# Kernel optimization log

Measured on AMD Instinct MI355X. Metric: run time of the kernel, lower is better.

The kernel has to match this reference:

```python
import jax, jax.numpy as jnp
import numpy as np

TW = 25; HID = 128; LAYERS = 6; SPATIAL = 1; NVAR = 1
TMAX = 4.0; TMIN = 0.0; RES_T = 250.0; DOM = 16.0
N = 65536; B = 8; E = 393216
EPS = 1e-5


def swish(x):
    return x * jax.nn.sigmoid(x)


def _forward(u, x_pos, t_pos, variables,
             emb_w1, emb_b1, emb_w2, emb_b2,
             m1_w, m1_b, m2_w, m2_b,
             u1_w, u1_b, u2_w, u2_b,
             c1_w, c1_b, c2_w, c2_b,
             edge_index, batch):
    t_norm = t_pos / TMAX                       # [N]
    pos = x_pos / DOM                           # [N, 1] normalized by domain extent
    node_in = jnp.concatenate([u, pos, t_norm[:, None], variables], axis=-1)
    f = swish(node_in @ emb_w1 + emb_b1)
    f = swish(f @ emb_w2 + emb_b2)              # [N, HID]

    var_all = jnp.concatenate([t_norm[:, None], variables], axis=-1)  # [N, NVAR+1]
    src, dst = edge_index[0], edge_index[1]     # PyG: x_j = x[src], x_i = x[dst]
    du = u[dst] - u[src]                        # [E, TW]
    dp = pos[dst] - pos[src]                    # [E, SPATIAL]
    v_i = var_all[dst]                          # [E, NVAR+1]

    ones_e = jnp.ones((E,), f.dtype)
    deg = jnp.maximum(jax.ops.segment_sum(ones_e, dst, num_segments=N), 1.0)
    ones_n = jnp.ones((N,), f.dtype)
    gcount = jnp.maximum(jax.ops.segment_sum(ones_n, batch, num_segments=B), 1.0)

    for l in range(LAYERS):
        # message: concat(x_i, x_j, u_i-u_j, pos_i-pos_j, vars_i) -> 2-layer MLP
        m = jnp.concatenate([f[dst], f[src], du, dp, v_i], axis=-1)  # [E, 284]
        m = swish(m @ m1_w[l] + m1_b[l])
        m = swish(m @ m2_w[l] + m2_b[l])
        agg = jax.ops.segment_sum(m, dst, num_segments=N) / deg[:, None]  # mean aggr
        # update: concat(x, message, vars) -> 2-layer MLP, residual (in==out)
        h = jnp.concatenate([f, agg, var_all], axis=-1)  # [N, 258]
        h = swish(h @ u1_w[l] + u1_b[l])
        h = swish(h @ u2_w[l] + u2_b[l])
        h = f + h
        # InstanceNorm over nodes within each graph, per feature (no affine)
        mean = jax.ops.segment_sum(h, batch, num_segments=B) / gcount[:, None]
        var = jax.ops.segment_sum(h * h, batch, num_segments=B) / gcount[:, None] - mean * mean
        f = (h - mean[batch]) * jax.lax.rsqrt(var[batch] + EPS)

    # output CNN head over feature axis: [N, 1, HID] -> [N, 1, TW]
    y = jax.lax.conv_general_dilated(f[:, None, :], c1_w, (3,), 'VALID',
                                     dimension_numbers=('NCH', 'OIH', 'NCH'))
    y = swish(y + c1_b[None, :, None])
    y = jax.lax.conv_general_dilated(y, c2_w, (1,), 'VALID',
                                     dimension_numbers=('NCH', 'OIH', 'NCH'))
    diff = y[:, 0, :] + c2_b[0]                 # [N, TW]

    dt = jnp.cumsum(jnp.full((TW,), (TMAX - TMIN) / RES_T, dtype=f.dtype))
    out = u[:, -1][:, None] + dt[None, :] * diff
    return out


def setup_inputs() -> dict:
    key = jax.random.key(0)
    keys = iter(jax.random.split(key, 128))

    def lin(i, o):
        s = 1.0 / np.sqrt(i)
        w = jax.random.uniform(next(keys), (i, o), jnp.float32, -s, s)
        b = jax.random.uniform(next(keys), (o,), jnp.float32, -s, s)
        return w, b

    def stacked(i, o):
        ws, bs = zip(*[lin(i, o) for _ in range(LAYERS)])
        return jnp.stack(ws), jnp.stack(bs)

    def conv(o, i, k):
        s = 1.0 / np.sqrt(i * k)
        w = jax.random.uniform(next(keys), (o, i, k), jnp.float32, -s, s)
        b = jax.random.uniform(next(keys), (o,), jnp.float32, -s, s)
        return w, b

    emb_w1, emb_b1 = lin(TW + SPATIAL + 1 + NVAR, HID)
    emb_w2, emb_b2 = lin(HID, HID)
    m1_w, m1_b = stacked(2 * HID + TW + SPATIAL + NVAR + 1, HID)
    m2_w, m2_b = stacked(HID, HID)
    u1_w, u1_b = stacked(2 * HID + NVAR + 1, HID)
    u2_w, u2_b = stacked(HID, HID)
    c1_w, c1_b = conv(8, 1, 16)
    c2_w, c2_b = conv(1, 8, 14)

    u = jax.random.normal(next(keys), (N, TW), jnp.float32)
    x_pos = jax.random.uniform(next(keys), (N, SPATIAL), jnp.float32) * DOM
    t_pos = jax.random.uniform(next(keys), (N,), jnp.float32) * TMAX
    variables = jax.random.normal(next(keys), (N, NVAR), jnp.float32)
    edge_index = jax.random.randint(next(keys), (2, E), 0, N, jnp.int32)
    batch = jnp.sort(jax.random.randint(next(keys), (N,), 0, B, jnp.int32))

    return {'u': u, 'x_pos': x_pos, 't_pos': t_pos, 'variables': variables,
            'edge_index': edge_index, 'batch': batch,
            'emb_w1': emb_w1, 'emb_b1': emb_b1, 'emb_w2': emb_w2, 'emb_b2': emb_b2,
            'm1_w': m1_w, 'm1_b': m1_b, 'm2_w': m2_w, 'm2_b': m2_b,
            'u1_w': u1_w, 'u1_b': u1_b, 'u2_w': u2_w, 'u2_b': u2_b,
            'c1_w': c1_w, 'c1_b': c1_b, 'c2_w': c2_w, 'c2_b': c2_b}


def reference(u, x_pos, t_pos, variables, edge_index, batch,
              emb_w1, emb_b1, emb_w2, emb_b2,
              m1_w, m1_b, m2_w, m2_b,
              u1_w, u1_b, u2_w, u2_b,
              c1_w, c1_b, c2_w, c2_b):
    return _forward(u, x_pos, t_pos, variables,
                    emb_w1, emb_b1, emb_w2, emb_b2,
                    m1_w, m1_b, m2_w, m2_b,
                    u1_w, u1_b, u2_w, u2_b,
                    c1_w, c1_b, c2_w, c2_b,
                    edge_index, batch)
```

## Files before the change

kernel.cpp:

```cpp
#include <hip/hip_runtime.h>
#include <hip/hip_bf16.h>

#define N_NODES 65536
#define N_EDGES 393216
#define NB 8
#define HID 128
#define TW 25
#define LAYERS 6
#define BGRAPH 8
#define EPSF 1e-5f
#define TILE_E 128

typedef __attribute__((ext_vector_type(8))) short bf16x8;
typedef __attribute__((ext_vector_type(4))) float f32x4;

__device__ __forceinline__ float swishf(float x) {
    return x / (1.0f + __expf(-x));
}

__device__ __forceinline__ unsigned short f2bf(float x) {
    unsigned int u = __float_as_uint(x);
    u += 0x7fffu + ((u >> 16) & 1u);
    return (unsigned short)(u >> 16);
}

__device__ __forceinline__ unsigned int cvtpk2bf(float lo, float hi) {
    unsigned int r;
    asm("v_cvt_pk_bf16_f32 %0, %1, %2" : "=v"(r) : "v"(lo), "v"(hi));
    return r;
}

__device__ __forceinline__ unsigned short f2bf_rne(float x) {
    unsigned int r;
    asm("v_cvt_pk_bf16_f32 %0, %1, %2" : "=v"(r) : "v"(x), "v"(x));
    return (unsigned short)r;
}

__device__ __forceinline__ float bf2f(unsigned short v) {
    return __uint_as_float(((unsigned int)v) << 16);
}

__global__ void gcount_kernel(const int* __restrict__ batch, float* __restrict__ gcount) {
    int b = threadIdx.x;
    if (b >= BGRAPH) return;
    auto lb = [&](int key) {
        int lo = 0, hi = N_NODES;
        while (lo < hi) { int mid = (lo + hi) >> 1; if (batch[mid] < key) lo = mid + 1; else hi = mid; }
        return lo;
    };
    int c = lb(b + 1) - lb(b);
    gcount[b] = c > 0 ? (float)c : 1.0f;
}

__global__ void count_kernel(const int* __restrict__ ei, int* __restrict__ cnt) {
    int e = blockIdx.x * 256 + threadIdx.x;
    if (e < N_EDGES) atomicAdd(&cnt[ei[N_EDGES + e]], 1);
}

__global__ __launch_bounds__(256) void block_sum_kernel(const int* __restrict__ cnt, int* __restrict__ bsum) {
    __shared__ int s[256];
    int t = threadIdx.x;
    s[t] = cnt[blockIdx.x * 256 + t];
    __syncthreads();
    for (int st = 128; st > 0; st >>= 1) {
        if (t < st) s[t] += s[t + st];
        __syncthreads();
    }
    if (t == 0) bsum[blockIdx.x] = s[0];
}

__global__ __launch_bounds__(256) void scan_bsum_kernel(const int* __restrict__ bsum, int* __restrict__ bpref) {
    __shared__ int s[256];
    int t = threadIdx.x;
    int orig = bsum[t];
    s[t] = orig;
    __syncthreads();
    for (int st = 1; st < 256; st <<= 1) {
        int v = (t >= st) ? s[t - st] : 0;
        __syncthreads();
        s[t] += v;
        __syncthreads();
    }
    bpref[t] = s[t] - orig;
}

__global__ __launch_bounds__(256) void offsets_kernel(const int* __restrict__ cnt, const int* __restrict__ bpref,
                                                      int* __restrict__ cursor) {
    __shared__ int s[256];
    int t = threadIdx.x;
    int base = blockIdx.x * 256;
    int orig = cnt[base + t];
    s[t] = orig;
    __syncthreads();
    for (int st = 1; st < 256; st <<= 1) {
        int v = (t >= st) ? s[t - st] : 0;
        __syncthreads();
        s[t] += v;
        __syncthreads();
    }
    cursor[base + t] = s[t] - orig + bpref[blockIdx.x];
}

__global__ void scatter_kernel(const int* __restrict__ ei, int* __restrict__ cursor,
                               int* __restrict__ src_s, int* __restrict__ dst_s) {
    int e = blockIdx.x * 256 + threadIdx.x;
    if (e >= N_EDGES) return;
    int d = ei[N_EDGES + e];
    int pos = atomicAdd(&cursor[d], 1);
    src_s[pos] = ei[e];
    dst_s[pos] = d;
}

__global__ void w2bf_kernel(const float* __restrict__ m2_w, unsigned short* __restrict__ W2T) {
    int idx = blockIdx.x * 256 + threadIdx.x;
    int l = idx >> 14;
    int rem = idx & 16383;
    int n = rem >> 7, k = rem & 127;
    W2T[idx] = f2bf(m2_w[l * 16384 + k * HID + n]);
}

__global__ void w1t_kernel(const float* __restrict__ m1_w, unsigned short* __restrict__ wAB) {
    int idx = blockIdx.x * 256 + threadIdx.x;
    int l = idx / (2 * 128 * 160);
    int rem = idx % (2 * 128 * 160);
    int pass = rem / (128 * 160);
    int o = (rem % (128 * 160)) / 160;
    int k = rem % 160;
    const float* M = m1_w + (size_t)l * 284 * 128;
    float v;
    if (k < 128) {
        v = M[(pass ? 128 + k : k) * 128 + o];
    } else {
        int ku = k - 128;
        if (ku < 25) v = M[(256 + ku) * 128 + o];
        else if (ku == 25) v = M[281 * 128 + o];
        else if (ku == 26) v = M[282 * 128 + o];
        else if (ku == 27) v = M[283 * 128 + o];
        else v = 0.0f;
        if (pass) v = (ku <= 25) ? -v : 0.0f;
    }
    wAB[idx] = f2bf(v);
}

__global__ void u1t_kernel(const float* __restrict__ u1_w, unsigned short* __restrict__ U1T) {
    int idx = blockIdx.x * 256 + threadIdx.x;
    int l = idx >> 15;
    int o = (idx >> 8) & 127;
    int k = idx & 255;
    U1T[idx] = f2bf(u1_w[(size_t)l * 258 * 128 + k * 128 + o]);
}

__global__ void u2t_kernel(const float* __restrict__ u2_w, unsigned short* __restrict__ U2T) {
    int idx = blockIdx.x * 256 + threadIdx.x;
    int l = idx >> 14;
    int o = (idx >> 7) & 127;
    int k = idx & 127;
    U2T[idx] = f2bf(u2_w[(size_t)l * 16384 + k * 128 + o]);
}

__global__ void wemb_kernel(const float* __restrict__ ew1, const float* __restrict__ ew2,
                            unsigned short* __restrict__ we1T, unsigned short* __restrict__ we2T) {
    int idx = blockIdx.x * 256 + threadIdx.x;
    if (idx < 4096) {
        int o = idx >> 5, k = idx & 31;
        we1T[idx] = f2bf(k < 28 ? ew1[k * HID + o] : 0.0f);
    } else {
        int j = idx - 4096;
        int o = j >> 7, k = j & 127;
        we2T[j] = f2bf(ew2[k * HID + o]);
    }
}

__global__ void xin_kernel(const float* __restrict__ u, const float* __restrict__ xpos,
                           const float* __restrict__ tpos, const float* __restrict__ vars,
                           unsigned short* __restrict__ xin) {
    int idx = blockIdx.x * 256 + threadIdx.x;
    int n = idx >> 5, k = idx & 31;
    float v;
    if (k < 25) v = u[n * TW + k];
    else if (k == 25) v = xpos[n] * (1.0f / 16.0f);
    else if (k == 26) v = tpos[n] * 0.25f;
    else if (k == 27) v = vars[n];
    else v = 0.0f;
    xin[idx] = f2bf(v);
}

__device__ __forceinline__ void abv_tail(
    const bf16x8 (&afr)[2][5], int nb, int lr, int lk,
    const unsigned short* __restrict__ wA, const unsigned short* __restrict__ wB,
    const float* __restrict__ b1,
    unsigned short* __restrict__ A_bf, unsigned short* __restrict__ Bv_bf)
{
    #pragma unroll 1
    for (int pass = 0; pass < 2; ++pass) {
        const unsigned short* Wp = pass ? wB : wA;
        unsigned short* Op = pass ? Bv_bf : A_bf;
        #pragma unroll 1
        for (int cc = 0; cc < 4; ++cc) {
            f32x4 acc[2][2];
            #pragma unroll
            for (int rt = 0; rt < 2; ++rt)
                #pragma unroll
                for (int cf2 = 0; cf2 < 2; ++cf2)
                    acc[rt][cf2] = (f32x4){0.0f, 0.0f, 0.0f, 0.0f};
            #pragma unroll
            for (int cf2 = 0; cf2 < 2; ++cf2) {
                const unsigned short* wrow = Wp + ((cc * 2 + cf2) * 16 + lr) * 160 + lk * 8;
                #pragma unroll
                for (int ks = 0; ks < 5; ++ks) {
                    bf16x8 bfr = *reinterpret_cast<const bf16x8*>(wrow + ks * 32);
                    acc[0][cf2] = __builtin_amdgcn_mfma_f32_16x16x32_bf16(afr[0][ks], bfr, acc[0][cf2], 0, 0, 0);
                    acc[1][cf2] = __builtin_amdgcn_mfma_f32_16x16x32_bf16(afr[1][ks], bfr, acc[1][cf2], 0, 0, 0);
                }
            }
            #pragma unroll
            for (int cf2 = 0; cf2 < 2; ++cf2) {
                int col = (cc * 2 + cf2) * 16 + lr;
                float bb = pass ? 0.0f : b1[col];
                #pragma unroll
                for (int rt = 0; rt < 2; ++rt) {
                    #pragma unroll
                    for (int j = 0; j < 4; ++j) {
                        int row = nb + rt * 16 + lk * 4 + j;
                        Op[(size_t)row * HID + col] = f2bf_rne(acc[rt][cf2][j] + bb);
                    }
                }
            }
        }
    }
}

__global__ __launch_bounds__(256) void emb_abv_kernel(
    const unsigned short* __restrict__ xin_bf,
    const unsigned short* __restrict__ we1T, const float* __restrict__ eb1,
    const unsigned short* __restrict__ we2T, const float* __restrict__ eb2,
    const unsigned short* __restrict__ wA, const unsigned short* __restrict__ wB,
    const float* __restrict__ b1,
    unsigned short* __restrict__ f_bf,
    unsigned short* __restrict__ A_bf, unsigned short* __restrict__ Bv_bf)
{
    __shared__ unsigned short q_lds[4 * 32 * HID];
    const int tid = threadIdx.x;
    const int w = tid >> 6, l = tid & 63;
    const int lr = l & 15, lk = l >> 4;
    const int nb = blockIdx.x * 128 + w * 32;
    char* qbase = reinterpret_cast<char*>(q_lds) + w * 8192;

    bf16x8 xfr[2];
    #pragma unroll
    for (int rt = 0; rt < 2; ++rt)
        xfr[rt] = *reinterpret_cast<const bf16x8*>(xin_bf + (size_t)(nb + rt * 16 + lr) * 32 + lk * 8);

    #pragma unroll 1
    for (int cc = 0; cc < 4; ++cc) {
        f32x4 acc1[2][2];
        #pragma unroll
        for (int rt = 0; rt < 2; ++rt)
            #pragma unroll
            for (int cf2 = 0; cf2 < 2; ++cf2)
                acc1[rt][cf2] = (f32x4){0.0f, 0.0f, 0.0f, 0.0f};
        #pragma unroll
        for (int cf2 = 0; cf2 < 2; ++cf2) {
            bf16x8 bfr = *reinterpret_cast<const bf16x8*>(we1T + ((cc * 2 + cf2) * 16 + lr) * 32 + lk * 8);
            acc1[0][cf2] = __builtin_amdgcn_mfma_f32_16x16x32_bf16(xfr[0], bfr, acc1[0][cf2], 0, 0, 0);
            acc1[1][cf2] = __builtin_amdgcn_mfma_f32_16x16x32_bf16(xfr[1], bfr, acc1[1][cf2], 0, 0, 0);
        }
        #pragma unroll
        for (int cf2 = 0; cf2 < 2; ++cf2) {
            int col = (cc * 2 + cf2) * 16 + lr;
            float bb = eb1[col];
            #pragma unroll
            for (int rt = 0; rt < 2; ++rt)
                #pragma unroll
                for (int j = 0; j < 4; ++j) {
                    float qv = swishf(acc1[rt][cf2][j] + bb);
                    int rloc = rt * 16 + lk * 4 + j;
                    *reinterpret_cast<unsigned short*>(qbase + rloc * 256 + ((col * 2) ^ ((rloc & 7) << 4))) = f2bf_rne(qv);
                }
        }
    }

    __shared__ unsigned short f_lds[4 * 32 * HID];
    char* fbase = reinterpret_cast<char*>(f_lds) + w * 8192;
    #pragma unroll 1
    for (int cc = 0; cc < 4; ++cc) {
        f32x4 acc2[2][2];
        #pragma unroll
        for (int rt = 0; rt < 2; ++rt)
            #pragma unroll
            for (int cf2 = 0; cf2 < 2; ++cf2)
                acc2[rt][cf2] = (f32x4){0.0f, 0.0f, 0.0f, 0.0f};
        #pragma unroll
        for (int ks = 0; ks < 4; ++ks) {
            bf16x8 afrq[2];
            #pragma unroll
            for (int rt = 0; rt < 2; ++rt) {
                int rloc = rt * 16 + lr;
                afrq[rt] = *reinterpret_cast<const bf16x8*>(qbase + rloc * 256 + ((ks * 64 + lk * 16) ^ ((rloc & 7) << 4)));
            }
            #pragma unroll
            for (int cf2 = 0; cf2 < 2; ++cf2) {
                bf16x8 bfr = *reinterpret_cast<const bf16x8*>(we2T + ((cc * 2 + cf2) * 16 + lr) * HID + ks * 32 + lk * 8);
                acc2[0][cf2] = __builtin_amdgcn_mfma_f32_16x16x32_bf16(afrq[0], bfr, acc2[0][cf2], 0, 0, 0);
                acc2[1][cf2] = __builtin_amdgcn_mfma_f32_16x16x32_bf16(afrq[1], bfr, acc2[1][cf2], 0, 0, 0);
            }
        }
        #pragma unroll
        for (int cf2 = 0; cf2 < 2; ++cf2) {
            int col = (cc * 2 + cf2) * 16 + lr;
            float bb = eb2[col];
            #pragma unroll
            for (int rt = 0; rt < 2; ++rt)
                #pragma unroll
                for (int j = 0; j < 4; ++j) {
                    float fv = swishf(acc2[rt][cf2][j] + bb);
                    unsigned short fb = f2bf_rne(fv);
                    int rloc = rt * 16 + lk * 4 + j;
                    f_bf[(size_t)(nb + rloc) * HID + col] = fb;
                    *reinterpret_cast<unsigned short*>(fbase + rloc * 256 + ((col * 2) ^ ((rloc & 7) << 4))) = fb;
                }
        }
    }

    bf16x8 afr[2][5];
    #pragma unroll
    for (int rt = 0; rt < 2; ++rt) {
        int rloc = rt * 16 + lr;
        #pragma unroll
        for (int ks = 0; ks < 4; ++ks)
            afr[rt][ks] = *reinterpret_cast<const bf16x8*>(fbase + rloc * 256 + ((ks * 64 + lk * 16) ^ ((rloc & 7) << 4)));
        afr[rt][4] = xfr[rt];
    }
    abv_tail(afr, nb, lr, lk, wA, wB, b1, A_bf, Bv_bf);
}

__global__ __launch_bounds__(256) void norm_abv_kernel(
    const unsigned short* __restrict__ h, const int* __restrict__ batch,
    const float* __restrict__ dsum, const float* __restrict__ dsq,
    const float* __restrict__ gcount,
    const unsigned short* __restrict__ xin_bf,
    const unsigned short* __restrict__ wA, const unsigned short* __restrict__ wB,
    const float* __restrict__ b1,
    unsigned short* __restrict__ f_bf,
    unsigned short* __restrict__ A_bf, unsigned short* __restrict__ Bv_bf)
{
    const int tid = threadIdx.x;
    const int w = tid >> 6, l = tid & 63;
    const int lr = l & 15, lk = l >> 4;
    const int nb = blockIdx.x * 128 + w * 32;

    bf16x8 afr[2][5];
    #pragma unroll
    for (int rt = 0; rt < 2; ++rt) {
        int row = nb + rt * 16 + lr;
        int b = batch[row];
        float inv = 1.0f / gcount[b];
        #pragma unroll
        for (int ks = 0; ks < 4; ++ks) {
            int c0 = ks * 32 + lk * 8;
            uint4 hv4 = *reinterpret_cast<const uint4*>(h + (size_t)row * HID + c0);
            unsigned int hw[4] = {hv4.x, hv4.y, hv4.z, hv4.w};
            float4 s0 = *reinterpret_cast<const float4*>(dsum + b * HID + c0);
            float4 s1 = *reinterpret_cast<const float4*>(dsum + b * HID + c0 + 4);
            float4 q0 = *reinterpret_cast<const float4*>(dsq + b * HID + c0);
            float4 q1 = *reinterpret_cast<const float4*>(dsq + b * HID + c0 + 4);
            float o[8];
            #pragma unroll
            for (int i = 0; i < 8; ++i) {
                float hx = (i & 1) ? __uint_as_float(hw[i >> 1] & 0xffff0000u)
                                   : __uint_as_float(hw[i >> 1] << 16);
                float sm = (i < 4) ? reinterpret_cast<const float*>(&s0)[i] : reinterpret_cast<const float*>(&s1)[i - 4];
                float sq = (i < 4) ? reinterpret_cast<const float*>(&q0)[i] : reinterpret_cast<const float*>(&q1)[i - 4];
                float mean = sm * inv;
                float var = sq * inv - mean * mean;
                o[i] = (hx - mean) * rsqrtf(var + EPSF);
            }
            union { bf16x8 v; unsigned int u[4]; } t;
            t.u[0] = cvtpk2bf(o[0], o[1]);
            t.u[1] = cvtpk2bf(o[2], o[3]);
            t.u[2] = cvtpk2bf(o[4], o[5]);
            t.u[3] = cvtpk2bf(o[6], o[7]);
            afr[rt][ks] = t.v;
            *reinterpret_cast<uint4*>(f_bf + (size_t)row * HID + c0) =
                *reinterpret_cast<const uint4*>(&t.v);
        }
        afr[rt][4] = *reinterpret_cast<const bf16x8*>(xin_bf + (size_t)row * 32 + lk * 8);
    }
    abv_tail(afr, nb, lr, lk, wA, wB, b1, A_bf, Bv_bf);
}

__global__ __launch_bounds__(256) void edge_mfma_kernel(
    const int* __restrict__ src_s, const int* __restrict__ dst_s,
    const unsigned short* __restrict__ A_bf, const unsigned short* __restrict__ Bv_bf,
    const unsigned short* __restrict__ W2T, const float* __restrict__ b2,
    float* __restrict__ agg)
{
    const int tid = threadIdx.x;
    const int w = tid >> 6, l = tid & 63;
    const int lr = l & 15, lk = l >> 4;
    const int e0 = blockIdx.x * TILE_E + w * 32;

    bf16x8 afr[2][4];
    #pragma unroll
    for (int rt = 0; rt < 2; ++rt) {
        int e = e0 + ((lr >> 2) << 3) + rt * 4 + (lr & 3);
        int dn = dst_s[e], sn = src_s[e];
        const unsigned short* ap = A_bf + (size_t)dn * HID + lk * 8;
        const unsigned short* bp = Bv_bf + (size_t)sn * HID + lk * 8;
        #pragma unroll
        for (int ks = 0; ks < 4; ++ks) {
            uint4 av = *reinterpret_cast<const uint4*>(ap + ks * 32);
            uint4 bv = *reinterpret_cast<const uint4*>(bp + ks * 32);
            auto proc = [](unsigned int aw, unsigned int bw) -> unsigned int {
                float a0 = __uint_as_float(aw << 16), a1 = __uint_as_float(aw & 0xffff0000u);
                float b0 = __uint_as_float(bw << 16), b1 = __uint_as_float(bw & 0xffff0000u);
                return cvtpk2bf(swishf(a0 + b0), swishf(a1 + b1));
            };
            union { bf16x8 v; unsigned int u[4]; } t;
            t.u[0] = proc(av.x, bv.x);
            t.u[1] = proc(av.y, bv.y);
            t.u[2] = proc(av.z, bv.z);
            t.u[3] = proc(av.w, bv.w);
            afr[rt][ks] = t.v;
        }
    }

    const int ebase = e0 + lk * 8;
    int4 dA4 = *reinterpret_cast<const int4*>(dst_s + ebase);
    int4 dB4 = *reinterpret_cast<const int4*>(dst_s + ebase + 4);
    int d[8] = {dA4.x, dA4.y, dA4.z, dA4.w, dB4.x, dB4.y, dB4.z, dB4.w};
    bool sm[7];
    int roff[8];
    #pragma unroll
    for (int m = 0; m < 7; ++m) sm[m] = (d[m + 1] == d[m]);
    #pragma unroll
    for (int m = 0; m < 8; ++m) roff[m] = d[m] * HID;

    #pragma unroll 1
    for (int cc = 0; cc < 4; ++cc) {
        f32x4 acc[2][2];
        #pragma unroll
        for (int rt = 0; rt < 2; ++rt)
            #pragma unroll
            for (int cf2 = 0; cf2 < 2; ++cf2)
                acc[rt][cf2] = (f32x4){0.0f, 0.0f, 0.0f, 0.0f};
        #pragma unroll
        for (int cf2 = 0; cf2 < 2; ++cf2) {
            const unsigned short* wrow = W2T + ((cc * 2 + cf2) * 16 + lr) * HID + lk * 8;
            #pragma unroll
            for (int ks = 0; ks < 4; ++ks) {
                bf16x8 bfr = *reinterpret_cast<const bf16x8*>(wrow + ks * 32);
                acc[0][cf2] = __builtin_amdgcn_mfma_f32_16x16x32_bf16(afr[0][ks], bfr, acc[0][cf2], 0, 0, 0);
                acc[1][cf2] = __builtin_amdgcn_mfma_f32_16x16x32_bf16(afr[1][ks], bfr, acc[1][cf2], 0, 0, 0);
            }
        }
        #pragma unroll
        for (int cf2 = 0; cf2 < 2; ++cf2) {
            int col = (cc * 2 + cf2) * 16 + lr;
            float bias = b2[col];
            float v[8];
            #pragma unroll
            for (int m = 0; m < 8; ++m) v[m] = swishf(acc[m >> 2][cf2][m & 3] + bias);
            float run = v[0];
            #pragma unroll
            for (int m = 1; m < 8; ++m) {
                if (sm[m - 1]) run += v[m];
                else { atomicAdd(&agg[(size_t)roff[m - 1] + col], run); run = v[m]; }
            }
            atomicAdd(&agg[(size_t)roff[7] + col], run);
        }
    }
}

__global__ __launch_bounds__(256) void update_mfma_kernel(
    const unsigned short* __restrict__ f_bf, const float* __restrict__ agg,
    const int* __restrict__ cnt,
    const float* __restrict__ tpos, const float* __restrict__ vars,
    const int* __restrict__ batch,
    const unsigned short* __restrict__ U1T, const float* __restrict__ u1tv,
    const float* __restrict__ b1, const unsigned short* __restrict__ U2T,
    const float* __restrict__ b2, unsigned short* __restrict__ h,
    float* __restrict__ dsum, float* __restrict__ dsq)
{
    __shared__ unsigned short q_lds[4 * 32 * HID];
    const int tid = threadIdx.x;
    const int w = tid >> 6, l = tid & 63;
    const int lr = l & 15, lk = l >> 4;
    const int nb = blockIdx.x * 128 + w * 32;
    char* qbase = reinterpret_cast<char*>(q_lds) + w * 8192;

    float invd[2];
    #pragma unroll
    for (int rt = 0; rt < 2; ++rt) {
        int c = cnt[nb + rt * 16 + lr];
        invd[rt] = 1.0f / (float)(c > 0 ? c : 1);
    }
    float tn[2][4], vn[2][4];
    #pragma unroll
    for (int rt = 0; rt < 2; ++rt)
        #pragma unroll
        for (int j = 0; j < 4; ++j) {
            int row = nb + rt * 16 + lk * 4 + j;
            tn[rt][j] = tpos[row] * 0.25f;
            vn[rt][j] = vars[row];
        }

    #pragma unroll 1
    for (int cc = 0; cc < 4; ++cc) {
        f32x4 acc[2][2];
        #pragma unroll
        for (int rt = 0; rt < 2; ++rt)
            #pragma unroll
            for (int cf2 = 0; cf2 < 2; ++cf2)
                acc[rt][cf2] = (f32x4){0.0f, 0.0f, 0.0f, 0.0f};
        #pragma unroll
        for (int ks = 0; ks < 8; ++ks) {
            bf16x8 afr[2];
            #pragma unroll
            for (int rt = 0; rt < 2; ++rt) {
                int row = nb + rt * 16 + lr;
                if (ks < 4) {
                    afr[rt] = *reinterpret_cast<const bf16x8*>(f_bf + (size_t)row * HID + ks * 32 + lk * 8);
                } else {
                    const float* ap = agg + (size_t)row * HID + (ks - 4) * 32 + lk * 8;
                    float4 a0 = *reinterpret_cast<const float4*>(ap);
                    float4 a1 = *reinterpret_cast<const float4*>(ap + 4);
                    float iv = invd[rt];
                    union { bf16x8 v; unsigned int u[4]; } t;
                    t.u[0] = cvtpk2bf(a0.x * iv, a0.y * iv);
                    t.u[1] = cvtpk2bf(a0.z * iv, a0.w * iv);
                    t.u[2] = cvtpk2bf(a1.x * iv, a1.y * iv);
                    t.u[3] = cvtpk2bf(a1.z * iv, a1.w * iv);
                    afr[rt] = t.v;
                }
            }
            #pragma unroll
            for (int cf2 = 0; cf2 < 2; ++cf2) {
                bf16x8 bfr = *reinterpret_cast<const bf16x8*>(U1T + ((cc * 2 + cf2) * 16 + lr) * 256 + ks * 32 + lk * 8);
                acc[0][cf2] = __builtin_amdgcn_mfma_f32_16x16x32_bf16(afr[0], bfr, acc[0][cf2], 0, 0, 0);
                acc[1][cf2] = __builtin_amdgcn_mfma_f32_16x16x32_bf16(afr[1], bfr, acc[1][cf2], 0, 0, 0);
            }
        }
        #pragma unroll
        for (int cf2 = 0; cf2 < 2; ++cf2) {
            int col = (cc * 2 + cf2) * 16 + lr;
            float bb = b1[col], wt = u1tv[col], wv = u1tv[HID + col];
            #pragma unroll
            for (int rt = 0; rt < 2; ++rt)
                #pragma unroll
                for (int j = 0; j < 4; ++j) {
                    float qv = swishf(acc[rt][cf2][j] + bb + tn[rt][j] * wt + vn[rt][j] * wv);
                    int rloc = rt * 16 + lk * 4 + j;
                    *reinterpret_cast<unsigned short*>(qbase + rloc * 256 + ((col * 2) ^ ((rloc & 7) << 4))) = f2bf_rne(qv);
                }
        }
    }

    const int bfirst = batch[nb];
    const bool uni = (bfirst == batch[nb + 31]);
    #pragma unroll 1
    for (int cc = 0; cc < 4; ++cc) {
        f32x4 acc2[2][2];
        #pragma unroll
        for (int rt = 0; rt < 2; ++rt)
            #pragma unroll
            for (int cf2 = 0; cf2 < 2; ++cf2)
                acc2[rt][cf2] = (f32x4){0.0f, 0.0f, 0.0f, 0.0f};
        #pragma unroll
        for (int ks = 0; ks < 4; ++ks) {
            bf16x8 afr[2];
            #pragma unroll
            for (int rt = 0; rt < 2; ++rt) {
                int rloc = rt * 16 + lr;
                afr[rt] = *reinterpret_cast<const bf16x8*>(qbase + rloc * 256 + ((ks * 64 + lk * 16) ^ ((rloc & 7) << 4)));
            }
            #pragma unroll
            for (int cf2 = 0; cf2 < 2; ++cf2) {
                bf16x8 bfr = *reinterpret_cast<const bf16x8*>(U2T + ((cc * 2 + cf2) * 16 + lr) * HID + ks * 32 + lk * 8);
                acc2[0][cf2] = __builtin_amdgcn_mfma_f32_16x16x32_bf16(afr[0], bfr, acc2[0][cf2], 0, 0, 0);
                acc2[1][cf2] = __builtin_amdgcn_mfma_f32_16x16x32_bf16(afr[1], bfr, acc2[1][cf2], 0, 0, 0);
            }
        }
        #pragma unroll
        for (int cf2 = 0; cf2 < 2; ++cf2) {
            int col = (cc * 2 + cf2) * 16 + lr;
            float bb = b2[col];
            float s = 0.0f, s2 = 0.0f;
            #pragma unroll
            for (int rt = 0; rt < 2; ++rt)
                #pragma unroll
                for (int j = 0; j < 4; ++j) {
                    int row = nb + rt * 16 + lk * 4 + j;
                    float fres = bf2f(f_bf[(size_t)row * HID + col]);
                    float hv = fres + swishf(acc2[rt][cf2][j] + bb);
                    unsigned short hb = f2bf_rne(hv);
                    h[(size_t)row * HID + col] = hb;
                    float hvr = bf2f(hb);
                    if (uni) { s += hvr; s2 += hvr * hvr; }
                    else {
                        int b = batch[row];
                        atomicAdd(&dsum[b * HID + col], hvr);
                        atomicAdd(&dsq[b * HID + col], hvr * hvr);
                    }
                }
            if (uni) {
                s += __shfl_xor(s, 16); s += __shfl_xor(s, 32);
                s2 += __shfl_xor(s2, 16); s2 += __shfl_xor(s2, 32);
                if (lk == 0) {
                    atomicAdd(&dsum[bfirst * HID + col], s);
                    atomicAdd(&dsq[bfirst * HID + col], s2);
                }
            }
        }
    }
}

__global__ __launch_bounds__(256) void head_kernel(
    const unsigned short* __restrict__ h, const int* __restrict__ batch,
    const float* __restrict__ dsum, const float* __restrict__ dsq,
    const float* __restrict__ gcount,
    const float* __restrict__ u,
    const float* __restrict__ c1w, const float* __restrict__ c1b,
    const float* __restrict__ c2w, const float* __restrict__ c2b,
    float* __restrict__ out)
{
    __shared__ float fs[16][HID];
    __shared__ float y1[16][8][40];
    const int tid = threadIdx.x;
    const int n0 = blockIdx.x * 16;
    {
        int node = tid >> 4, cb = tid & 15;
        int n = n0 + node;
        int b = batch[n];
        float inv = 1.0f / gcount[b];
        int c0 = cb * 8;
        uint4 v = *reinterpret_cast<const uint4*>(h + (size_t)n * HID + c0);
        unsigned int wv[4] = {v.x, v.y, v.z, v.w};
        #pragma unroll
        for (int i = 0; i < 8; ++i) {
            float hx = (i & 1) ? __uint_as_float(wv[i >> 1] & 0xffff0000u)
                               : __uint_as_float(wv[i >> 1] << 16);
            float mean = dsum[b * HID + c0 + i] * inv;
            float var = dsq[b * HID + c0 + i] * inv - mean * mean;
            fs[node][c0 + i] = (hx - mean) * rsqrtf(var + EPSF);
        }
    }
    __syncthreads();
    {
        const int node = tid >> 4;
        const int rem = tid & 15;
        const int o = rem >> 1;
        const int ph = rem & 1;
        const float cb = c1b[o];
        float wk[16];
        #pragma unroll
        for (int k = 0; k < 16; ++k) wk[k] = c1w[o * 16 + k];
        for (int p = ph * 19; p < ph * 19 + 19; ++p) {
            float acc = cb;
            #pragma unroll
            for (int k = 0; k < 16; ++k) acc += fs[node][p * 3 + k] * wk[k];
            y1[node][o][p] = swishf(acc);
        }
    }
    __syncthreads();
    const float cb2 = c2b[0];
    #pragma unroll
    for (int pass = 0; pass < 2; ++pass) {
        int unit = tid + pass * 256;
        if (unit < 16 * TW) {
            int node = unit / TW, t = unit % TW;
            float acc = cb2;
            #pragma unroll
            for (int o = 0; o < 8; ++o)
                #pragma unroll
                for (int k = 0; k < 14; ++k)
                    acc += y1[node][o][t + k] * c2w[o * 14 + k];
            int n = n0 + node;
            out[n * TW + t] = u[n * TW + (TW - 1)] + (0.016f * (float)(t + 1)) * acc;
        }
    }
}

extern "C" void kernel_launch(void* const* d_in, const int* in_sizes, int n_in,
                              void* d_out, int out_size, void* d_ws, size_t ws_size,
                              hipStream_t stream)
{
    (void)in_sizes; (void)n_in; (void)out_size; (void)ws_size;
    const float* u      = (const float*)d_in[0];
    const float* xpos   = (const float*)d_in[1];
    const float* tpos   = (const float*)d_in[2];
    const float* vars   = (const float*)d_in[3];
    const int*   ei     = (const int*)d_in[4];
    const int*   batch  = (const int*)d_in[5];
    const float* emb_w1 = (const float*)d_in[6];
    const float* emb_b1 = (const float*)d_in[7];
    const float* emb_w2 = (const float*)d_in[8];
    const float* emb_b2 = (const float*)d_in[9];
    const float* m1_w   = (const float*)d_in[10];
    const float* m1_b   = (const float*)d_in[11];
    const float* m2_w   = (const float*)d_in[12];
    const float* m2_b   = (const float*)d_in[13];
    const float* u1_w   = (const float*)d_in[14];
    const float* u1_b   = (const float*)d_in[15];
    const float* u2_w   = (const float*)d_in[16];
    const float* u2_b   = (const float*)d_in[17];
    const float* c1w    = (const float*)d_in[18];
    const float* c1b    = (const float*)d_in[19];
    const float* c2w    = (const float*)d_in[20];
    const float* c2b    = (const float*)d_in[21];
    float* out = (float*)d_out;

    char* ws = (char*)d_ws;
    const size_t fbytes = (size_t)N_NODES * HID * sizeof(float);
    float* agg    = (float*)(ws);
    char*  p      = ws + fbytes;
    unsigned short* h_bf   = (unsigned short*)p;  p += (size_t)N_NODES * HID * 2;
    unsigned short* A_bf   = (unsigned short*)p;  p += (size_t)N_NODES * HID * 2;
    unsigned short* Bv_bf  = (unsigned short*)p;  p += (size_t)N_NODES * HID * 2;
    unsigned short* f_bf   = (unsigned short*)p;  p += (size_t)N_NODES * HID * 2;
    unsigned short* xin_bf = (unsigned short*)p;  p += (size_t)N_NODES * 32 * 2;
    int* cnt      = (int*)p;               p += (size_t)N_NODES * 4;
    int* cursor   = (int*)p;               p += (size_t)N_NODES * 4;
    int* src_s    = (int*)p;               p += (size_t)N_EDGES * 4;
    int* dst_s    = (int*)p;               p += (size_t)N_EDGES * 4;
    int* bsum     = (int*)p;               p += 256 * 4;
    int* bpref    = (int*)p;               p += 256 * 4;
    float* dsumL  = (float*)p;             p += (size_t)LAYERS * BGRAPH * HID * 4;
    float* dsqL   = (float*)p;             p += (size_t)LAYERS * BGRAPH * HID * 4;
    float* gcount = (float*)p;             p += BGRAPH * 4;
    unsigned short* W2T  = (unsigned short*)p;  p += (size_t)LAYERS * HID * HID * 2;
    unsigned short* wAB  = (unsigned short*)p;  p += (size_t)LAYERS * 2 * 128 * 160 * 2;
    unsigned short* U1T  = (unsigned short*)p;  p += (size_t)LAYERS * 128 * 256 * 2;
    unsigned short* U2T  = (unsigned short*)p;  p += (size_t)LAYERS * 128 * 128 * 2;
    unsigned short* we1T = (unsigned short*)p;  p += 128 * 32 * 2;
    unsigned short* we2T = (unsigned short*)p;  p += 128 * 128 * 2;

    hipMemsetAsync(cnt, 0, (size_t)N_NODES * 4, stream);
    count_kernel<<<N_EDGES / 256, 256, 0, stream>>>(ei, cnt);
    block_sum_kernel<<<N_NODES / 256, 256, 0, stream>>>(cnt, bsum);
    scan_bsum_kernel<<<1, 256, 0, stream>>>(bsum, bpref);
    offsets_kernel<<<N_NODES / 256, 256, 0, stream>>>(cnt, bpref, cursor);
    scatter_kernel<<<N_EDGES / 256, 256, 0, stream>>>(ei, cursor, src_s, dst_s);

    w2bf_kernel<<<LAYERS * HID * HID / 256, 256, 0, stream>>>(m2_w, W2T);
    w1t_kernel<<<LAYERS * 2 * 128 * 160 / 256, 256, 0, stream>>>(m1_w, wAB);
    u1t_kernel<<<LAYERS * 128 * 256 / 256, 256, 0, stream>>>(u1_w, U1T);
    u2t_kernel<<<LAYERS * 128 * 128 / 256, 256, 0, stream>>>(u2_w, U2T);
    wemb_kernel<<<80, 256, 0, stream>>>(emb_w1, emb_w2, we1T, we2T);
    xin_kernel<<<N_NODES * 32 / 256, 256, 0, stream>>>(u, xpos, tpos, vars, xin_bf);
    gcount_kernel<<<1, 64, 0, stream>>>(batch, gcount);
    hipMemsetAsync(dsumL, 0, (size_t)2 * LAYERS * BGRAPH * HID * 4, stream);

    emb_abv_kernel<<<N_NODES / 128, 256, 0, stream>>>(
        xin_bf, we1T, emb_b1, we2T, emb_b2,
        wAB, wAB + 128 * 160, m1_b, f_bf, A_bf, Bv_bf);

    for (int l = 0; l < LAYERS; ++l) {
        hipMemsetAsync(agg, 0, fbytes, stream);
        edge_mfma_kernel<<<N_EDGES / TILE_E, 256, 0, stream>>>(
            src_s, dst_s, A_bf, Bv_bf, W2T + (size_t)l * HID * HID,
            m2_b + (size_t)l * HID, agg);
        update_mfma_kernel<<<N_NODES / 128, 256, 0, stream>>>(
            f_bf, agg, cnt, tpos, vars, batch,
            U1T + (size_t)l * 128 * 256,
            u1_w + (size_t)l * 258 * 128 + 256 * 128,
            u1_b + (size_t)l * HID,
            U2T + (size_t)l * 128 * 128,
            u2_b + (size_t)l * HID, h_bf,
            dsumL + (size_t)l * BGRAPH * HID, dsqL + (size_t)l * BGRAPH * HID);
        if (l < LAYERS - 1) {
            norm_abv_kernel<<<N_NODES / 128, 256, 0, stream>>>(
                h_bf, batch, dsumL + (size_t)l * BGRAPH * HID, dsqL + (size_t)l * BGRAPH * HID,
                gcount, xin_bf,
                wAB + (size_t)(l + 1) * 2 * 128 * 160,
                wAB + (size_t)(l + 1) * 2 * 128 * 160 + 128 * 160,
                m1_b + (size_t)(l + 1) * HID,
                f_bf, A_bf, Bv_bf);
        }
    }
    head_kernel<<<N_NODES / 16, 256, 0, stream>>>(
        h_bf, batch, dsumL + (size_t)(LAYERS - 1) * BGRAPH * HID,
        dsqL + (size_t)(LAYERS - 1) * BGRAPH * HID, gcount,
        u, c1w, c1b, c2w, c2b, out);
}
```

Baseline: 1.399 ms.

## Split node-kernel output columns across waves with shared LDS tiles

```diff
diff --git a/kernel.cpp b/kernel.cpp
--- a/kernel.cpp
+++ b/kernel.cpp
@@ -185,46 +185,37 @@
     xin[idx] = f2bf(v);
 }
 
-__device__ __forceinline__ void abv_tail(
-    const bf16x8 (&afr)[2][5], int nb, int lr, int lk,
-    const unsigned short* __restrict__ wA, const unsigned short* __restrict__ wB,
-    const float* __restrict__ b1,
-    unsigned short* __restrict__ A_bf, unsigned short* __restrict__ Bv_bf)
+__device__ __forceinline__ void abv_chunk(
+    const bf16x8 (&afr)[2][5], int nb, int lr, int lk, int colbase,
+    const unsigned short* __restrict__ Wp, const float* __restrict__ b1,
+    unsigned short* __restrict__ Op)
 {
-    #pragma unroll 1
-    for (int pass = 0; pass < 2; ++pass) {
-        const unsigned short* Wp = pass ? wB : wA;
-        unsigned short* Op = pass ? Bv_bf : A_bf;
-        #pragma unroll 1
-        for (int cc = 0; cc < 4; ++cc) {
-            f32x4 acc[2][2];
-            #pragma unroll
-            for (int rt = 0; rt < 2; ++rt)
-                #pragma unroll
-                for (int cf2 = 0; cf2 < 2; ++cf2)
-                    acc[rt][cf2] = (f32x4){0.0f, 0.0f, 0.0f, 0.0f};
-            #pragma unroll
-            for (int cf2 = 0; cf2 < 2; ++cf2) {
-                const unsigned short* wrow = Wp + ((cc * 2 + cf2) * 16 + lr) * 160 + lk * 8;
-                #pragma unroll
-                for (int ks = 0; ks < 5; ++ks) {
-                    bf16x8 bfr = *reinterpret_cast<const bf16x8*>(wrow + ks * 32);
-                    acc[0][cf2] = __builtin_amdgcn_mfma_f32_16x16x32_bf16(afr[0][ks], bfr, acc[0][cf2], 0, 0, 0);
-                    acc[1][cf2] = __builtin_amdgcn_mfma_f32_16x16x32_bf16(afr[1][ks], bfr, acc[1][cf2], 0, 0, 0);
-                }
-            }
-            #pragma unroll
-            for (int cf2 = 0; cf2 < 2; ++cf2) {
-                int col = (cc * 2 + cf2) * 16 + lr;
-                float bb = pass ? 0.0f : b1[col];
-                #pragma unroll
-                for (int rt = 0; rt < 2; ++rt) {
-                    #pragma unroll
-                    for (int j = 0; j < 4; ++j) {
-                        int row = nb + rt * 16 + lk * 4 + j;
-                        Op[(size_t)row * HID + col] = f2bf_rne(acc[rt][cf2][j] + bb);
-                    }
-                }
+    f32x4 acc[2][2];
+    #pragma unroll
+    for (int rt = 0; rt < 2; ++rt)
+        #pragma unroll
+        for (int cf2 = 0; cf2 < 2; ++cf2)
+            acc[rt][cf2] = (f32x4){0.0f, 0.0f, 0.0f, 0.0f};
+    #pragma unroll
+    for (int cf2 = 0; cf2 < 2; ++cf2) {
+        const unsigned short* wrow = Wp + (colbase + cf2 * 16 + lr) * 160 + lk * 8;
+        #pragma unroll
+        for (int ks = 0; ks < 5; ++ks) {
+            bf16x8 bfr = *reinterpret_cast<const bf16x8*>(wrow + ks * 32);
+            acc[0][cf2] = __builtin_amdgcn_mfma_f32_16x16x32_bf16(afr[0][ks], bfr, acc[0][cf2], 0, 0, 0);
+            acc[1][cf2] = __builtin_amdgcn_mfma_f32_16x16x32_bf16(afr[1][ks], bfr, acc[1][cf2], 0, 0, 0);
+        }
+    }
+    #pragma unroll
+    for (int cf2 = 0; cf2 < 2; ++cf2) {
+        int col = colbase + cf2 * 16 + lr;
+        float bb = b1 ? b1[col] : 0.0f;
+        #pragma unroll
+        for (int rt = 0; rt < 2; ++rt) {
+            #pragma unroll
+            for (int j = 0; j < 4; ++j) {
+                int row = nb + rt * 16 + lk * 4 + j;
+                Op[(size_t)row * HID + col] = f2bf_rne(acc[rt][cf2][j] + bb);
             }
         }
     }
@@ -280,8 +271,8 @@
         }
     }
 
-    __shared__ unsigned short f_lds[4 * 32 * HID];
-    char* fbase = reinterpret_cast<char*>(f_lds) + w * 8192;
+    __shared__ unsigned short f_lds2[4 * 32 * HID];
+    char* fbase = reinterpret_cast<char*>(f_lds2) + w * 8192;
     #pragma unroll 1
     for (int cc = 0; cc < 4; ++cc) {
         f32x4 acc2[2][2];
@@ -331,7 +322,10 @@
             afr[rt][ks] = *reinterpret_cast<const bf16x8*>(fbase + rloc * 256 + ((ks * 64 + lk * 16) ^ ((rloc & 7) << 4)));
         afr[rt][4] = xfr[rt];
     }
-    abv_tail(afr, nb, lr, lk, wA, wB, b1, A_bf, Bv_bf);
+    #pragma unroll 1
+    for (int cc = 0; cc < 4; ++cc) abv_chunk(afr, nb, lr, lk, cc * 32, wA, b1, A_bf);
+    #pragma unroll 1
+    for (int cc = 0; cc < 4; ++cc) abv_chunk(afr, nb, lr, lk, cc * 32, wB, nullptr, Bv_bf);
 }
 
 __global__ __launch_bounds__(256) void norm_abv_kernel(
@@ -344,20 +338,20 @@
     unsigned short* __restrict__ f_bf,
     unsigned short* __restrict__ A_bf, unsigned short* __restrict__ Bv_bf)
 {
+    __shared__ unsigned short f_lds[32 * HID];
     const int tid = threadIdx.x;
     const int w = tid >> 6, l = tid & 63;
     const int lr = l & 15, lk = l >> 4;
-    const int nb = blockIdx.x * 128 + w * 32;
-
-    bf16x8 afr[2][5];
-    #pragma unroll
-    for (int rt = 0; rt < 2; ++rt) {
-        int row = nb + rt * 16 + lr;
-        int b = batch[row];
-        float inv = 1.0f / gcount[b];
-        #pragma unroll
-        for (int ks = 0; ks < 4; ++ks) {
-            int c0 = ks * 32 + lk * 8;
+    const int nb = blockIdx.x * 32;
+
+    {
+        const int ks = w;
+        const int c0 = ks * 32 + lk * 8;
+        #pragma unroll
+        for (int rt = 0; rt < 2; ++rt) {
+            int row = nb + rt * 16 + lr;
+            int b = batch[row];
+            float inv = 1.0f / gcount[b];
             uint4 hv4 = *reinterpret_cast<const uint4*>(h + (size_t)row * HID + c0);
             unsigned int hw[4] = {hv4.x, hv4.y, hv4.z, hv4.w};
             float4 s0 = *reinterpret_cast<const float4*>(dsum + b * HID + c0);
@@ -375,18 +369,30 @@
                 float var = sq * inv - mean * mean;
                 o[i] = (hx - mean) * rsqrtf(var + EPSF);
             }
-            union { bf16x8 v; unsigned int u[4]; } t;
-            t.u[0] = cvtpk2bf(o[0], o[1]);
-            t.u[1] = cvtpk2bf(o[2], o[3]);
-            t.u[2] = cvtpk2bf(o[4], o[5]);
-            t.u[3] = cvtpk2bf(o[6], o[7]);
-            afr[rt][ks] = t.v;
-            *reinterpret_cast<uint4*>(f_bf + (size_t)row * HID + c0) =
-                *reinterpret_cast<const uint4*>(&t.v);
-        }
-        afr[rt][4] = *reinterpret_cast<const bf16x8*>(xin_bf + (size_t)row * 32 + lk * 8);
-    }
-    abv_tail(afr, nb, lr, lk, wA, wB, b1, A_bf, Bv_bf);
+            uint4 t;
+            t.x = cvtpk2bf(o[0], o[1]);
+            t.y = cvtpk2bf(o[2], o[3]);
+            t.z = cvtpk2bf(o[4], o[5]);
+            t.w = cvtpk2bf(o[6], o[7]);
+            *reinterpret_cast<uint4*>(f_bf + (size_t)row * HID + c0) = t;
+            int rloc = rt * 16 + lr;
+            *reinterpret_cast<uint4*>(reinterpret_cast<char*>(f_lds) + rloc * 256 + ((c0 * 2) ^ ((rloc & 7) << 4))) = t;
+        }
+    }
+    __syncthreads();
+
+    bf16x8 afr[2][5];
+    #pragma unroll
+    for (int rt = 0; rt < 2; ++rt) {
+        int rloc = rt * 16 + lr;
+        #pragma unroll
+        for (int ks = 0; ks < 4; ++ks)
+            afr[rt][ks] = *reinterpret_cast<const bf16x8*>(
+                reinterpret_cast<const char*>(f_lds) + rloc * 256 + ((ks * 64 + lk * 16) ^ ((rloc & 7) << 4)));
+        afr[rt][4] = *reinterpret_cast<const bf16x8*>(xin_bf + (size_t)(nb + rt * 16 + lr) * 32 + lk * 8);
+    }
+    abv_chunk(afr, nb, lr, lk, w * 32, wA, b1, A_bf);
+    abv_chunk(afr, nb, lr, lk, w * 32, wB, nullptr, Bv_bf);
 }
 
 __global__ __launch_bounds__(256) void edge_mfma_kernel(
@@ -482,12 +488,11 @@
     const float* __restrict__ b2, unsigned short* __restrict__ h,
     float* __restrict__ dsum, float* __restrict__ dsq)
 {
-    __shared__ unsigned short q_lds[4 * 32 * HID];
+    __shared__ unsigned short q_lds[32 * HID];
     const int tid = threadIdx.x;
     const int w = tid >> 6, l = tid & 63;
     const int lr = l & 15, lk = l >> 4;
-    const int nb = blockIdx.x * 128 + w * 32;
-    char* qbase = reinterpret_cast<char*>(q_lds) + w * 8192;
+    const int nb = blockIdx.x * 32;
 
     float invd[2];
     #pragma unroll
@@ -505,8 +510,7 @@
             vn[rt][j] = vars[row];
         }
 
-    #pragma unroll 1
-    for (int cc = 0; cc < 4; ++cc) {
+    {
         f32x4 acc[2][2];
         #pragma unroll
         for (int rt = 0; rt < 2; ++rt)
@@ -536,14 +540,14 @@
             }
             #pragma unroll
             for (int cf2 = 0; cf2 < 2; ++cf2) {
-                bf16x8 bfr = *reinterpret_cast<const bf16x8*>(U1T + ((cc * 2 + cf2) * 16 + lr) * 256 + ks * 32 + lk * 8);
+                bf16x8 bfr = *reinterpret_cast<const bf16x8*>(U1T + ((w * 2 + cf2) * 16 + lr) * 256 + ks * 32 + lk * 8);
                 acc[0][cf2] = __builtin_amdgcn_mfma_f32_16x16x32_bf16(afr[0], bfr, acc[0][cf2], 0, 0, 0);
                 acc[1][cf2] = __builtin_amdgcn_mfma_f32_16x16x32_bf16(afr[1], bfr, acc[1][cf2], 0, 0, 0);
             }
         }
         #pragma unroll
         for (int cf2 = 0; cf2 < 2; ++cf2) {
-            int col = (cc * 2 + cf2) * 16 + lr;
+            int col = w * 32 + cf2 * 16 + lr;
             float bb = b1[col], wt = u1tv[col], wv = u1tv[HID + col];
             #pragma unroll
             for (int rt = 0; rt < 2; ++rt)
@@ -551,15 +555,15 @@
                 for (int j = 0; j < 4; ++j) {
                     float qv = swishf(acc[rt][cf2][j] + bb + tn[rt][j] * wt + vn[rt][j] * wv);
                     int rloc = rt * 16 + lk * 4 + j;
-                    *reinterpret_cast<unsigned short*>(qbase + rloc * 256 + ((col * 2) ^ ((rloc & 7) << 4))) = f2bf_rne(qv);
+                    *reinterpret_cast<unsigned short*>(reinterpret_cast<char*>(q_lds) + rloc * 256 + ((col * 2) ^ ((rloc & 7) << 4))) = f2bf_rne(qv);
                 }
         }
     }
+    __syncthreads();
 
     const int bfirst = batch[nb];
     const bool uni = (bfirst == batch[nb + 31]);
-    #pragma unroll 1
-    for (int cc = 0; cc < 4; ++cc) {
+    {
         f32x4 acc2[2][2];
         #pragma unroll
         for (int rt = 0; rt < 2; ++rt)
@@ -572,18 +576,19 @@
             #pragma unroll
             for (int rt = 0; rt < 2; ++rt) {
                 int rloc = rt * 16 + lr;
-                afr[rt] = *reinterpret_cast<const bf16x8*>(qbase + rloc * 256 + ((ks * 64 + lk * 16) ^ ((rloc & 7) << 4)));
+                afr[rt] = *reinterpret_cast<const bf16x8*>(
+                    reinterpret_cast<const char*>(q_lds) + rloc * 256 + ((ks * 64 + lk * 16) ^ ((rloc & 7) << 4)));
             }
             #pragma unroll
             for (int cf2 = 0; cf2 < 2; ++cf2) {
-                bf16x8 bfr = *reinterpret_cast<const bf16x8*>(U2T + ((cc * 2 + cf2) * 16 + lr) * HID + ks * 32 + lk * 8);
+                bf16x8 bfr = *reinterpret_cast<const bf16x8*>(U2T + ((w * 2 + cf2) * 16 + lr) * HID + ks * 32 + lk * 8);
                 acc2[0][cf2] = __builtin_amdgcn_mfma_f32_16x16x32_bf16(afr[0], bfr, acc2[0][cf2], 0, 0, 0);
                 acc2[1][cf2] = __builtin_amdgcn_mfma_f32_16x16x32_bf16(afr[1], bfr, acc2[1][cf2], 0, 0, 0);
             }
         }
         #pragma unroll
         for (int cf2 = 0; cf2 < 2; ++cf2) {
-            int col = (cc * 2 + cf2) * 16 + lr;
+            int col = w * 32 + cf2 * 16 + lr;
             float bb = b2[col];
             float s = 0.0f, s2 = 0.0f;
             #pragma unroll
@@ -760,7 +765,7 @@
         edge_mfma_kernel<<<N_EDGES / TILE_E, 256, 0, stream>>>(
             src_s, dst_s, A_bf, Bv_bf, W2T + (size_t)l * HID * HID,
             m2_b + (size_t)l * HID, agg);
-        update_mfma_kernel<<<N_NODES / 128, 256, 0, stream>>>(
+        update_mfma_kernel<<<N_NODES / 32, 256, 0, stream>>>(
             f_bf, agg, cnt, tpos, vars, batch,
             U1T + (size_t)l * 128 * 256,
             u1_w + (size_t)l * 258 * 128 + 256 * 128,
@@ -769,7 +774,7 @@
             u2_b + (size_t)l * HID, h_bf,
             dsumL + (size_t)l * BGRAPH * HID, dsqL + (size_t)l * BGRAPH * HID);
         if (l < LAYERS - 1) {
-            norm_abv_kernel<<<N_NODES / 128, 256, 0, stream>>>(
+            norm_abv_kernel<<<N_NODES / 32, 256, 0, stream>>>(
                 h_bf, batch, dsumL + (size_t)l * BGRAPH * HID, dsqL + (size_t)l * BGRAPH * HID,
                 gcount, xin_bf,
                 wAB + (size_t)(l + 1) * 2 * 128 * 160,
```

New measurement: 1.205 ms. -13.9%, faster.
